# Performance work log

Measured on AMD Instinct MI355X. Metric: run time of the kernel, lower is better.

The kernel has to match this reference:

```python
import jax, jax.numpy as jnp
import numpy as np

NCAMS, NIDENT = 160, 256
B, C, H, W = 32, 3, 1024, 1024


def setup_inputs() -> dict:
    key = jax.random.key(0)
    k_img, k_cam, k_id, k1, k2, k3, k4 = jax.random.split(key, 7)
    image = jax.random.normal(k_img, (B, C, H, W), dtype=jnp.float32)
    camindex = jax.random.randint(k_cam, (B,), 0, NCAMS)
    idindex = jax.random.randint(k_id, (B,), 0, NIDENT)
    # Learned per-camera / per-identity channel affine params.
    # Torch init is wcam=ones, others=zeros; perturb so the math is non-degenerate.
    wcam = 1.0 + 0.1 * jax.random.normal(k1, (NCAMS, 3), dtype=jnp.float32)
    bcam = 0.1 * jax.random.normal(k2, (NCAMS, 3), dtype=jnp.float32)
    wident = 0.1 * jax.random.normal(k3, (NIDENT, 3), dtype=jnp.float32)
    bident = 0.1 * jax.random.normal(k4, (NIDENT, 3), dtype=jnp.float32)
    return {"image": image, "camindex": camindex, "idindex": idindex,
            "wcam": wcam, "bcam": bcam, "wident": wident, "bident": bident}


def reference(image, camindex, idindex, wcam, bcam, wident, bident):
    # Batched gather of per-sample channel affine: w,b are [B,3]
    w = wcam[camindex] + wident[idindex]
    b = bcam[camindex] + bident[idindex]
    # Broadcast [B,3] -> [B,3,1,1] and apply fused scale+bias over [B,3,H,W]
    return w[:, :, None, None] * image + b[:, :, None, None]
```

## Files before the change

### kernel.cpp

```cpp
#include <hip/hip_runtime.h>
#include <hip/hip_bf16.h>


#define HW (1024 * 1024)
#define HW4 (HW / 4)

__global__ __launch_bounds__(256) void colorcal_kernel(
    const float* __restrict__ image,
    const int*   __restrict__ camindex,
    const int*   __restrict__ idindex,
    const float* __restrict__ wcam,
    const float* __restrict__ bcam,
    const float* __restrict__ wident,
    const float* __restrict__ bident,
    float* __restrict__ out)
{
    const int plane = blockIdx.y;
    const int b     = plane / 3;
    const int c     = plane - b * 3;

    const int cam = camindex[b];
    const int id  = idindex[b];
    const float w    = wcam[cam * 3 + c] + wident[id * 3 + c];
    const float bias = bcam[cam * 3 + c] + bident[id * 3 + c];

    const size_t planeBase = (size_t)plane * HW;
    const float4* __restrict__ in4  = reinterpret_cast<const float4*>(image + planeBase);
    float4*       __restrict__ out4 = reinterpret_cast<float4*>(out + planeBase);

    const int stride = gridDim.x * blockDim.x;
    for (int i = blockIdx.x * blockDim.x + threadIdx.x; i < HW4; i += stride) {
        float4 v = in4[i];
        v.x = fmaf(w, v.x, bias);
        v.y = fmaf(w, v.y, bias);
        v.z = fmaf(w, v.z, bias);
        v.w = fmaf(w, v.w, bias);
        out4[i] = v;
    }
}

extern "C" void kernel_launch(void* const* d_in, const int* in_sizes, int n_in,
                              void* d_out, int out_size, void* d_ws, size_t ws_size,
                              hipStream_t stream) {
    const float* image    = (const float*)d_in[0];
    const int*   camindex = (const int*)  d_in[1];
    const int*   idindex  = (const int*)  d_in[2];
    const float* wcam     = (const float*)d_in[3];
    const float* bcam     = (const float*)d_in[4];
    const float* wident   = (const float*)d_in[5];
    const float* bident   = (const float*)d_in[6];
    float* out = (float*)d_out;

    dim3 grid(128, 96, 1);
    dim3 block(256, 1, 1);
    colorcal_kernel<<<grid, block, 0, stream>>>(
        image, camindex, idindex, wcam, bcam, wident, bident, out);
}
```

Before: 159.9 us.

## Use nontemporal vector loads/stores with 4x unrolled loop and smaller grid

Replaces the grid-stride loop with a fixed-trip loop that issues four independent 16-byte nontemporal loads and stores per iteration, and shrinks the grid from 128 to 16 blocks per plane. The intent is to keep more memory requests in flight per thread and avoid polluting caches with streaming data. A smaller grid lowers block-scheduling overhead but relies on each thread's unrolled loads for latency hiding, and the loop bound now assumes HW is divisible by the stride.

```diff
diff --git a/kernel.cpp b/kernel.cpp
--- a/kernel.cpp
+++ b/kernel.cpp
@@ -2,8 +2,14 @@
 #include <hip/hip_bf16.h>
 
 
-#define HW (1024 * 1024)
-#define HW4 (HW / 4)
+typedef float f32x4 __attribute__((ext_vector_type(4)));
+
+#define HW     (1024 * 1024)
+#define HW4    (HW / 4)
+#define GRIDX  16
+#define TPB    256
+#define STRIDE (GRIDX * TPB)
+#define ITERS  (HW4 / (STRIDE * 4))
 
 __global__ __launch_bounds__(256) void colorcal_kernel(
     const float* __restrict__ image,
@@ -25,17 +31,27 @@
     const float bias = bcam[cam * 3 + c] + bident[id * 3 + c];
 
     const size_t planeBase = (size_t)plane * HW;
-    const float4* __restrict__ in4  = reinterpret_cast<const float4*>(image + planeBase);
-    float4*       __restrict__ out4 = reinterpret_cast<float4*>(out + planeBase);
+    const f32x4* __restrict__ in4  = reinterpret_cast<const f32x4*>(image + planeBase);
+    f32x4*       __restrict__ out4 = reinterpret_cast<f32x4*>(out + planeBase);
 
-    const int stride = gridDim.x * blockDim.x;
-    for (int i = blockIdx.x * blockDim.x + threadIdx.x; i < HW4; i += stride) {
-        float4 v = in4[i];
-        v.x = fmaf(w, v.x, bias);
-        v.y = fmaf(w, v.y, bias);
-        v.z = fmaf(w, v.z, bias);
-        v.w = fmaf(w, v.w, bias);
-        out4[i] = v;
+    const int tid = blockIdx.x * TPB + threadIdx.x;
+
+    for (int it = 0; it < ITERS; ++it) {
+        const int i0 = it * (STRIDE * 4) + tid;
+        f32x4 v0 = __builtin_nontemporal_load(&in4[i0 + 0 * STRIDE]);
+        f32x4 v1 = __builtin_nontemporal_load(&in4[i0 + 1 * STRIDE]);
+        f32x4 v2 = __builtin_nontemporal_load(&in4[i0 + 2 * STRIDE]);
+        f32x4 v3 = __builtin_nontemporal_load(&in4[i0 + 3 * STRIDE]);
+
+        v0 = v0 * w + bias;
+        v1 = v1 * w + bias;
+        v2 = v2 * w + bias;
+        v3 = v3 * w + bias;
+
+        __builtin_nontemporal_store(v0, &out4[i0 + 0 * STRIDE]);
+        __builtin_nontemporal_store(v1, &out4[i0 + 1 * STRIDE]);
+        __builtin_nontemporal_store(v2, &out4[i0 + 2 * STRIDE]);
+        __builtin_nontemporal_store(v3, &out4[i0 + 3 * STRIDE]);
     }
 }
 
@@ -51,8 +67,8 @@
     const float* bident   = (const float*)d_in[6];
     float* out = (float*)d_out;
 
-    dim3 grid(128, 96, 1);
-    dim3 block(256, 1, 1);
+    dim3 grid(GRIDX, 96, 1);
+    dim3 block(TPB, 1, 1);
     colorcal_kernel<<<grid, block, 0, stream>>>(
         image, camindex, idindex, wcam, bcam, wident, bident, out);
 }
```

Result: slower. 175.8 us (+9.9%).
